# Performance work log

Hardware: AMD Instinct MI355X
Metric: run time of the kernel (lower is better)

Reference implementation:

```python
import jax, jax.numpy as jnp
import numpy as np

N = 50000      # nodes
E = 640000     # edges
F_IN = 128     # dataset.num_features
DIM = 128      # mParams['dim']
NC = 6         # dataset.num_classes
BN_EPS = 1e-5


def _bn_eval(z, g, b, rm, rv):
    return g * (z - rm) * jax.lax.rsqrt(rv + BN_EPS) + b


def _gin_layer(h, src, dst, W1, b1, g, be, rm, rv, W2, b2):
    # GINConv (eps=0): nn(x + sum_{j->i} x_j); messages from src aggregated at dst
    agg = jax.ops.segment_sum(h[src], dst, num_segments=N)
    z = (h + agg) @ W1 + b1
    z = jax.nn.relu(_bn_eval(z, g, be, rm, rv))
    z = jax.nn.relu(z @ W2 + b2)
    return z


def setup_inputs() -> dict:
    key = jax.random.key(0)
    ks = jax.random.split(key, 10)
    s = 1.0 / np.sqrt(DIM)
    inp = {
        'x': jax.random.normal(ks[0], (N, F_IN), jnp.float32),
        'edge_index': jax.random.randint(ks[1], (2, E), 0, N, dtype=jnp.int32),
        'batch': jnp.zeros((N,), jnp.int32),
        # conv1 MLP: Linear(F_IN,DIM) -> BN(DIM) -> ReLU -> Linear(DIM,DIM) -> ReLU
        'c1_W1': jax.random.normal(ks[2], (F_IN, DIM), jnp.float32) * s,
        'c1_b1': jnp.zeros((DIM,), jnp.float32),
        'c1_g': jnp.ones((DIM,), jnp.float32),
        'c1_beta': jnp.zeros((DIM,), jnp.float32),
        'c1_rm': jnp.zeros((DIM,), jnp.float32),
        'c1_rv': jnp.ones((DIM,), jnp.float32),
        'c1_W2': jax.random.normal(ks[3], (DIM, DIM), jnp.float32) * s,
        'c1_b2': jnp.zeros((DIM,), jnp.float32),
        # 2 extra GINConv layers (c_depth-1), stacked on leading axis
        'conv_W1': jax.random.normal(ks[4], (2, DIM, DIM), jnp.float32) * s,
        'conv_b1': jnp.zeros((2, DIM), jnp.float32),
        'conv_g': jnp.ones((2, DIM), jnp.float32),
        'conv_beta': jnp.zeros((2, DIM), jnp.float32),
        'conv_rm': jnp.zeros((2, DIM), jnp.float32),
        'conv_rv': jnp.ones((2, DIM), jnp.float32),
        'conv_W2': jax.random.normal(ks[5], (2, DIM, DIM), jnp.float32) * s,
        'conv_b2': jnp.zeros((2, DIM), jnp.float32),
        # 2 linear layers (l_depth)
        'lin_W': jax.random.normal(ks[6], (2, DIM, DIM), jnp.float32) * s,
        'lin_b': jnp.zeros((2, DIM), jnp.float32),
        # classifier Linear(2*DIM, NC)
        'cls_W': jax.random.normal(ks[7], (2 * DIM, NC), jnp.float32) * s,
        'cls_b': jnp.zeros((NC,), jnp.float32),
    }
    return inp


def reference(x, edge_index, batch,
              c1_W1, c1_b1, c1_g, c1_beta, c1_rm, c1_rv, c1_W2, c1_b2,
              conv_W1, conv_b1, conv_g, conv_beta, conv_rm, conv_rv, conv_W2, conv_b2,
              lin_W, lin_b, cls_W, cls_b):
    src, dst = edge_index[0], edge_index[1]
    h = _gin_layer(x, src, dst, c1_W1, c1_b1, c1_g, c1_beta, c1_rm, c1_rv, c1_W2, c1_b2)
    h = jax.nn.relu(h)  # extra .relu() after conv1 (idempotent)
    for i in range(conv_W1.shape[0]):
        h = _gin_layer(h, src, dst, conv_W1[i], conv_b1[i], conv_g[i], conv_beta[i],
                       conv_rm[i], conv_rv[i], conv_W2[i], conv_b2[i])
        h = jax.nn.relu(h)
    for i in range(lin_W.shape[0]):
        h = jax.nn.relu(h @ lin_W[i] + lin_b[i])
    # dropout: eval mode -> identity
    e = jnp.concatenate([h[src], h[dst]], axis=1)  # [E, 2*DIM]
    out = e @ cls_W + cls_b                         # [E, NC]
    return (out, e)
```

## Files before the change

kernel.cpp:

```cpp
#include <hip/hip_runtime.h>
#include <cstddef>
#include <cstdint>

#define NN 50000
#define EE 640000
#define FD 128


__global__ __launch_bounds__(256) void k_zero(int* __restrict__ p) {
  int i = blockIdx.x * 256 + threadIdx.x;
  if (i < NN) p[i] = 0;
}

__global__ __launch_bounds__(256) void k_hist(const int* __restrict__ dst,
                                              int* __restrict__ deg) {
  int e = blockIdx.x * 256 + threadIdx.x;
  atomicAdd(&deg[dst[e]], 1);
}

__global__ __launch_bounds__(1024) void k_scan(const int* __restrict__ deg,
                                               int* __restrict__ off,
                                               int* __restrict__ cur) {
  __shared__ int wsum[16], woff[16];
  __shared__ int carryS;
  const int t = threadIdx.x, lane = t & 63, w = t >> 6;
  if (t == 0) carryS = 0;
  __syncthreads();
  for (int base = 0; base < NN; base += 4096) {
    int i = base + (t << 2);
    int4 dv = make_int4(0, 0, 0, 0);
    if (i < NN) dv = *reinterpret_cast<const int4*>(deg + i);
    int tsum = dv.x + dv.y + dv.z + dv.w;
    int incl = tsum;
#pragma unroll
    for (int d = 1; d < 64; d <<= 1) {
      int u = __shfl_up(incl, d, 64);
      if (lane >= d) incl += u;
    }
    if (lane == 63) wsum[w] = incl;
    __syncthreads();
    if (t == 0) {
      int run = 0;
#pragma unroll
      for (int k = 0; k < 16; ++k) { woff[k] = run; run += wsum[k]; }
    }
    __syncthreads();
    int ebase = (incl - tsum) + woff[w] + carryS;
    if (i < NN) {
      int4 ov;
      ov.x = ebase;
      ov.y = ebase + dv.x;
      ov.z = ov.y + dv.y;
      ov.w = ov.z + dv.z;
      *reinterpret_cast<int4*>(off + i) = ov;
      *reinterpret_cast<int4*>(cur + i) = ov;
    }
    __syncthreads();
    if (t == 0) carryS += woff[15] + wsum[15];
    __syncthreads();
  }
}

__global__ __launch_bounds__(256) void k_fill(const int* __restrict__ src,
                                              const int* __restrict__ dst,
                                              int* __restrict__ cur,
                                              int* __restrict__ ssrc) {
  int e = blockIdx.x * 256 + threadIdx.x;
  int d = dst[e];
  int pos = atomicAdd(&cur[d], 1);
  ssrc[pos] = src[e];
}

__global__ __launch_bounds__(256) void k_agg(const float* __restrict__ h,
                                             const int* __restrict__ off,
                                             const int* __restrict__ deg,
                                             const int* __restrict__ ssrc,
                                             float* __restrict__ agg) {
  int node = blockIdx.x * 8 + (threadIdx.x >> 5);
  int lane = threadIdx.x & 31;
  int f = lane << 2;
  float4 acc = *reinterpret_cast<const float4*>(h + (size_t)node * FD + f);
  int n = deg[node];
  const int* sl = ssrc + off[node];
  int j = 0;
  for (; j + 4 <= n; j += 4) {
    int s0 = sl[j], s1 = sl[j + 1], s2 = sl[j + 2], s3 = sl[j + 3];
    float4 v0 = *reinterpret_cast<const float4*>(h + (size_t)s0 * FD + f);
    float4 v1 = *reinterpret_cast<const float4*>(h + (size_t)s1 * FD + f);
    float4 v2 = *reinterpret_cast<const float4*>(h + (size_t)s2 * FD + f);
    float4 v3 = *reinterpret_cast<const float4*>(h + (size_t)s3 * FD + f);
    acc.x += (v0.x + v1.x) + (v2.x + v3.x);
    acc.y += (v0.y + v1.y) + (v2.y + v3.y);
    acc.z += (v0.z + v1.z) + (v2.z + v3.z);
    acc.w += (v0.w + v1.w) + (v2.w + v3.w);
  }
  for (; j < n; ++j) {
    int s = sl[j];
    float4 v = *reinterpret_cast<const float4*>(h + (size_t)s * FD + f);
    acc.x += v.x; acc.y += v.y; acc.z += v.z; acc.w += v.w;
  }
  *reinterpret_cast<float4*>(agg + (size_t)node * FD + f) = acc;
}

__global__ __launch_bounds__(256) void k_gemm(const float* __restrict__ A,
                                              const float* __restrict__ W,
                                              const float* __restrict__ bias,
                                              const float* __restrict__ gg,
                                              const float* __restrict__ bb,
                                              const float* __restrict__ rm,
                                              const float* __restrict__ rv,
                                              int use_bn,
                                              float* __restrict__ O, int M) {
  __shared__ float At[64][68];
  __shared__ float Ws[64][132];
  const int t  = threadIdx.x;
  const int tx = t & 15;
  const int ty = t >> 4;
  const int rowBase = blockIdx.x * 64;

  float acc[4][8] = {};

  for (int kc = 0; kc < 2; ++kc) {
    const int k0 = kc * 64;
#pragma unroll
    for (int i = 0; i < 4; ++i) {
      int idx = t + i * 256;
      int row = idx >> 4;
      int kg  = (idx & 15) << 2;
      int r = rowBase + row;
      float4 v = make_float4(0.f, 0.f, 0.f, 0.f);
      if (r < M) v = *reinterpret_cast<const float4*>(A + (size_t)r * FD + k0 + kg);
      At[kg + 0][row] = v.x;
      At[kg + 1][row] = v.y;
      At[kg + 2][row] = v.z;
      At[kg + 3][row] = v.w;
    }
#pragma unroll
    for (int i = 0; i < 8; ++i) {
      int idx = t + i * 256;
      int wr = idx >> 5;
      int wc = (idx & 31) << 2;
      *reinterpret_cast<float4*>(&Ws[wr][wc]) =
          *reinterpret_cast<const float4*>(W + (size_t)(k0 + wr) * FD + wc);
    }
    __syncthreads();

#pragma unroll 8
    for (int k = 0; k < 64; ++k) {
      const float4 a  = *reinterpret_cast<const float4*>(&At[k][ty << 2]);
      const float4 w0 = *reinterpret_cast<const float4*>(&Ws[k][tx << 3]);
      const float4 w1 = *reinterpret_cast<const float4*>(&Ws[k][(tx << 3) + 4]);
      const float av[4] = {a.x, a.y, a.z, a.w};
      const float wv[8] = {w0.x, w0.y, w0.z, w0.w, w1.x, w1.y, w1.z, w1.w};
#pragma unroll
      for (int i = 0; i < 4; ++i)
#pragma unroll
        for (int j = 0; j < 8; ++j)
          acc[i][j] = fmaf(av[i], wv[j], acc[i][j]);
    }
    __syncthreads();
  }

  const int c0 = tx << 3;
  float sc[8], sh[8];
#pragma unroll
  for (int j = 0; j < 8; ++j) {
    int c = c0 + j;
    if (use_bn) {
      float s = gg[c] * rsqrtf(rv[c] + 1e-5f);
      sc[j] = s;
      sh[j] = (bias[c] - rm[c]) * s + bb[c];
    } else {
      sc[j] = 1.f;
      sh[j] = bias[c];
    }
  }
#pragma unroll
  for (int i = 0; i < 4; ++i) {
    int r = rowBase + (ty << 2) + i;
    if (r < M) {
      float o[8];
#pragma unroll
      for (int j = 0; j < 8; ++j) {
        float v = fmaf(acc[i][j], sc[j], sh[j]);
        o[j] = v > 0.f ? v : 0.f;
      }
      *reinterpret_cast<float4*>(O + (size_t)r * FD + c0) =
          make_float4(o[0], o[1], o[2], o[3]);
      *reinterpret_cast<float4*>(O + (size_t)r * FD + c0 + 4) =
          make_float4(o[4], o[5], o[6], o[7]);
    }
  }
}

__global__ __launch_bounds__(256) void k_uv(const float* __restrict__ h,
                                            const float* __restrict__ clsW,
                                            float* __restrict__ U,
                                            float* __restrict__ V) {
  int t = blockIdx.x * 256 + threadIdx.x;
  int r = t / 12;
  int c = t % 12;
  if (r >= NN) return;
  int cc = (c < 6) ? c : c - 6;
  int base = (c < 6) ? 0 : FD;
  const float* hr = h + (size_t)r * FD;
  float acc = 0.f;
#pragma unroll 8
  for (int k = 0; k < FD; ++k)
    acc = fmaf(hr[k], clsW[(size_t)(base + k) * 6 + cc], acc);
  if (c < 6) U[(size_t)r * 6 + cc] = acc;
  else       V[(size_t)r * 6 + cc] = acc;
}

__global__ __launch_bounds__(256) void k_edge(const float* __restrict__ h,
                                              const int* __restrict__ src,
                                              const int* __restrict__ dst,
                                              const float* __restrict__ U,
                                              const float* __restrict__ V,
                                              const float* __restrict__ clsB,
                                              float* __restrict__ outL,
                                              float* __restrict__ outE) {
  int eid  = blockIdx.x * 4 + (threadIdx.x >> 6);
  int lane = threadIdx.x & 63;
  int s = src[eid];
  int d = dst[eid];
  int node = (lane < 32) ? s : d;
  int f = (lane & 31) << 2;
  float4 v = *reinterpret_cast<const float4*>(h + (size_t)node * FD + f);
  *reinterpret_cast<float4*>(outE + (size_t)eid * 256 + (lane << 2)) = v;
  if (lane < 6)
    outL[(size_t)eid * 6 + lane] = U[(size_t)s * 6 + lane] + V[(size_t)d * 6 + lane] + clsB[lane];
}

extern "C" void kernel_launch(void* const* d_in, const int* in_sizes, int n_in,
                              void* d_out, int out_size, void* d_ws, size_t ws_size,
                              hipStream_t stream) {
  const float* x     = (const float*)d_in[0];
  const int*   ei    = (const int*)d_in[1];
  const int*   src   = ei;
  const int*   dst   = ei + EE;
  const float* c1_W1 = (const float*)d_in[3];
  const float* c1_b1 = (const float*)d_in[4];
  const float* c1_g  = (const float*)d_in[5];
  const float* c1_be = (const float*)d_in[6];
  const float* c1_rm = (const float*)d_in[7];
  const float* c1_rv = (const float*)d_in[8];
  const float* c1_W2 = (const float*)d_in[9];
  const float* c1_b2 = (const float*)d_in[10];
  const float* cv_W1 = (const float*)d_in[11];
  const float* cv_b1 = (const float*)d_in[12];
  const float* cv_g  = (const float*)d_in[13];
  const float* cv_be = (const float*)d_in[14];
  const float* cv_rm = (const float*)d_in[15];
  const float* cv_rv = (const float*)d_in[16];
  const float* cv_W2 = (const float*)d_in[17];
  const float* cv_b2 = (const float*)d_in[18];
  const float* ln_W  = (const float*)d_in[19];
  const float* ln_b  = (const float*)d_in[20];
  const float* clsW  = (const float*)d_in[21];
  const float* clsB  = (const float*)d_in[22];

  float* buf0 = (float*)d_ws;
  float* buf1 = buf0 + (size_t)NN * FD;
  float* Uu   = buf1 + (size_t)NN * FD;
  float* Vv   = Uu + (size_t)NN * 6;

  float* outL = (float*)d_out;
  float* outE = outL + (size_t)EE * 6;

  const size_t outFloats = (size_t)EE * 262;
  const size_t scrInts   = (size_t)NN * 3 + (size_t)EE;
  const size_t scrStart  = (outFloats - scrInts) & ~(size_t)3;
  int* deg  = (int*)d_out + scrStart;
  int* off  = deg + NN;
  int* curp = off + NN;
  int* ssrc = curp + NN;

  dim3 B(256);
  const int gZero = (NN + 255) / 256;
  const int gEdgeWk = EE / 256;
  const int gAgg  = NN / 8;
  const int gGemm = (NN + 63) / 64;
  const int gUV   = (NN * 12 + 255) / 256;
  const int gEdge = EE / 4;

  k_zero<<<gZero, B, 0, stream>>>(deg);
  k_hist<<<gEdgeWk, B, 0, stream>>>(dst, deg);
  k_scan<<<1, dim3(1024), 0, stream>>>(deg, off, curp);
  k_fill<<<gEdgeWk, B, 0, stream>>>(src, dst, curp, ssrc);

  float* bufs[2] = {buf0, buf1};

  k_agg<<<gAgg, B, 0, stream>>>(x, off, deg, ssrc, buf0);
  k_gemm<<<gGemm, B, 0, stream>>>(buf0, c1_W1, c1_b1, c1_g, c1_be, c1_rm, c1_rv, 1, buf1, NN);
  k_gemm<<<gGemm, B, 0, stream>>>(buf1, c1_W2, c1_b2, nullptr, nullptr, nullptr, nullptr, 0, buf0, NN);
  int pp = 0;

  for (int l = 0; l < 2; ++l) {
    float* hc = bufs[pp];
    float* ho = bufs[1 - pp];
    k_agg<<<gAgg, B, 0, stream>>>(hc, off, deg, ssrc, ho);
    k_gemm<<<gGemm, B, 0, stream>>>(ho, cv_W1 + (size_t)l * FD * FD, cv_b1 + l * FD,
                                    cv_g + l * FD, cv_be + l * FD, cv_rm + l * FD,
                                    cv_rv + l * FD, 1, hc, NN);
    k_gemm<<<gGemm, B, 0, stream>>>(hc, cv_W2 + (size_t)l * FD * FD, cv_b2 + l * FD,
                                    nullptr, nullptr, nullptr, nullptr, 0, ho, NN);
    pp = 1 - pp;
  }

  for (int l = 0; l < 2; ++l) {
    k_gemm<<<gGemm, B, 0, stream>>>(bufs[pp], ln_W + (size_t)l * FD * FD, ln_b + l * FD,
                                    nullptr, nullptr, nullptr, nullptr, 0, bufs[1 - pp], NN);
    pp = 1 - pp;
  }

  k_uv<<<gUV, B, 0, stream>>>(bufs[pp], clsW, Uu, Vv);
  k_edge<<<gEdge, B, 0, stream>>>(bufs[pp], src, dst, Uu, Vv, clsB, outL, outE);
}
```

Measured before the change: 1.428 ms.

## Retile GEMM to 128-row blocks, warp-reduce classifier, unroll aggregation, nontemporal edge stores

The GEMM block tile grows from 64 to 128 rows with 8x8 register tiles per thread and 32-wide k chunks, which raises arithmetic intensity per shared-memory load. The U/V classifier projection now uses 32 lanes per node with coalesced float4 row reads and a shuffle reduction, replacing one thread per output that read the whole row serially. The aggregation loop gains an 8-way unrolled gather to put more loads in flight, and the large edge-feature output is written with nontemporal stores to reduce cache pollution. The larger register tile may lower occupancy, and the gather-heavy kernels remain limited by memory bandwidth.

```diff
diff --git a/kernel.cpp b/kernel.cpp
--- a/kernel.cpp
+++ b/kernel.cpp
@@ -5,6 +5,8 @@
 #define NN 50000
 #define EE 640000
 #define FD 128
+
+typedef float fvec4 __attribute__((ext_vector_type(4)));
 
 
 __global__ __launch_bounds__(256) void k_zero(int* __restrict__ p) {
@@ -83,6 +85,27 @@
   int n = deg[node];
   const int* sl = ssrc + off[node];
   int j = 0;
+  for (; j + 8 <= n; j += 8) {
+    int s0 = sl[j], s1 = sl[j + 1], s2 = sl[j + 2], s3 = sl[j + 3];
+    int s4 = sl[j + 4], s5 = sl[j + 5], s6 = sl[j + 6], s7 = sl[j + 7];
+    float4 v0 = *reinterpret_cast<const float4*>(h + (size_t)s0 * FD + f);
+    float4 v1 = *reinterpret_cast<const float4*>(h + (size_t)s1 * FD + f);
+    float4 v2 = *reinterpret_cast<const float4*>(h + (size_t)s2 * FD + f);
+    float4 v3 = *reinterpret_cast<const float4*>(h + (size_t)s3 * FD + f);
+    float4 v4 = *reinterpret_cast<const float4*>(h + (size_t)s4 * FD + f);
+    float4 v5 = *reinterpret_cast<const float4*>(h + (size_t)s5 * FD + f);
+    float4 v6 = *reinterpret_cast<const float4*>(h + (size_t)s6 * FD + f);
+    float4 v7 = *reinterpret_cast<const float4*>(h + (size_t)s7 * FD + f);
+    float tx0 = (v0.x + v1.x) + (v2.x + v3.x);
+    float ty0 = (v0.y + v1.y) + (v2.y + v3.y);
+    float tz0 = (v0.z + v1.z) + (v2.z + v3.z);
+    float tw0 = (v0.w + v1.w) + (v2.w + v3.w);
+    float tx1 = (v4.x + v5.x) + (v6.x + v7.x);
+    float ty1 = (v4.y + v5.y) + (v6.y + v7.y);
+    float tz1 = (v4.z + v5.z) + (v6.z + v7.z);
+    float tw1 = (v4.w + v5.w) + (v6.w + v7.w);
+    acc.x += tx0 + tx1; acc.y += ty0 + ty1; acc.z += tz0 + tz1; acc.w += tw0 + tw1;
+  }
   for (; j + 4 <= n; j += 4) {
     int s0 = sl[j], s1 = sl[j + 1], s2 = sl[j + 2], s3 = sl[j + 3];
     float4 v0 = *reinterpret_cast<const float4*>(h + (size_t)s0 * FD + f);
@@ -111,22 +134,22 @@
                                               const float* __restrict__ rv,
                                               int use_bn,
                                               float* __restrict__ O, int M) {
-  __shared__ float At[64][68];
-  __shared__ float Ws[64][132];
+  __shared__ float At[32][132];
+  __shared__ float Ws[32][132];
   const int t  = threadIdx.x;
   const int tx = t & 15;
   const int ty = t >> 4;
-  const int rowBase = blockIdx.x * 64;
-
-  float acc[4][8] = {};
-
-  for (int kc = 0; kc < 2; ++kc) {
-    const int k0 = kc * 64;
+  const int rowBase = blockIdx.x * 128;
+
+  float acc[8][8] = {};
+
+  for (int kc = 0; kc < 4; ++kc) {
+    const int k0 = kc << 5;
 #pragma unroll
     for (int i = 0; i < 4; ++i) {
-      int idx = t + i * 256;
-      int row = idx >> 4;
-      int kg  = (idx & 15) << 2;
+      int fl = t + (i << 8);
+      int row = fl & 127;
+      int kg  = (fl >> 7) << 2;
       int r = rowBase + row;
       float4 v = make_float4(0.f, 0.f, 0.f, 0.f);
       if (r < M) v = *reinterpret_cast<const float4*>(A + (size_t)r * FD + k0 + kg);
@@ -136,36 +159,36 @@
       At[kg + 3][row] = v.w;
     }
 #pragma unroll
-    for (int i = 0; i < 8; ++i) {
-      int idx = t + i * 256;
-      int wr = idx >> 5;
-      int wc = (idx & 31) << 2;
+    for (int i = 0; i < 4; ++i) {
+      int fl = t + (i << 8);
+      int wr = fl >> 5;
+      int wc = (fl & 31) << 2;
       *reinterpret_cast<float4*>(&Ws[wr][wc]) =
           *reinterpret_cast<const float4*>(W + (size_t)(k0 + wr) * FD + wc);
     }
     __syncthreads();
 
 #pragma unroll 8
-    for (int k = 0; k < 64; ++k) {
-      const float4 a  = *reinterpret_cast<const float4*>(&At[k][ty << 2]);
-      const float4 w0 = *reinterpret_cast<const float4*>(&Ws[k][tx << 3]);
-      const float4 w1 = *reinterpret_cast<const float4*>(&Ws[k][(tx << 3) + 4]);
-      const float av[4] = {a.x, a.y, a.z, a.w};
+    for (int k = 0; k < 32; ++k) {
+      const float4 a0 = *reinterpret_cast<const float4*>(&At[k][ty << 3]);
+      const float4 a1 = *reinterpret_cast<const float4*>(&At[k][(ty << 3) + 4]);
+      const float4 w0 = *reinterpret_cast<const float4*>(&Ws[k][tx << 2]);
+      const float4 w1 = *reinterpret_cast<const float4*>(&Ws[k][64 + (tx << 2)]);
+      const float av[8] = {a0.x, a0.y, a0.z, a0.w, a1.x, a1.y, a1.z, a1.w};
       const float wv[8] = {w0.x, w0.y, w0.z, w0.w, w1.x, w1.y, w1.z, w1.w};
 #pragma unroll
-      for (int i = 0; i < 4; ++i)
+      for (int i2 = 0; i2 < 8; ++i2)
 #pragma unroll
         for (int j = 0; j < 8; ++j)
-          acc[i][j] = fmaf(av[i], wv[j], acc[i][j]);
-    }
-    __syncthreads();
-  }
-
-  const int c0 = tx << 3;
+          acc[i2][j] = fmaf(av[i2], wv[j], acc[i2][j]);
+    }
+    __syncthreads();
+  }
+
   float sc[8], sh[8];
 #pragma unroll
   for (int j = 0; j < 8; ++j) {
-    int c = c0 + j;
+    int c = (j < 4) ? ((tx << 2) + j) : (64 + (tx << 2) + (j - 4));
     if (use_bn) {
       float s = gg[c] * rsqrtf(rv[c] + 1e-5f);
       sc[j] = s;
@@ -176,8 +199,8 @@
     }
   }
 #pragma unroll
-  for (int i = 0; i < 4; ++i) {
-    int r = rowBase + (ty << 2) + i;
+  for (int i = 0; i < 8; ++i) {
+    int r = rowBase + (ty << 3) + i;
     if (r < M) {
       float o[8];
 #pragma unroll
@@ -185,9 +208,9 @@
         float v = fmaf(acc[i][j], sc[j], sh[j]);
         o[j] = v > 0.f ? v : 0.f;
       }
-      *reinterpret_cast<float4*>(O + (size_t)r * FD + c0) =
+      *reinterpret_cast<float4*>(O + (size_t)r * FD + (tx << 2)) =
           make_float4(o[0], o[1], o[2], o[3]);
-      *reinterpret_cast<float4*>(O + (size_t)r * FD + c0 + 4) =
+      *reinterpret_cast<float4*>(O + (size_t)r * FD + 64 + (tx << 2)) =
           make_float4(o[4], o[5], o[6], o[7]);
     }
   }
@@ -197,19 +220,32 @@
                                             const float* __restrict__ clsW,
                                             float* __restrict__ U,
                                             float* __restrict__ V) {
-  int t = blockIdx.x * 256 + threadIdx.x;
-  int r = t / 12;
-  int c = t % 12;
-  if (r >= NN) return;
-  int cc = (c < 6) ? c : c - 6;
-  int base = (c < 6) ? 0 : FD;
-  const float* hr = h + (size_t)r * FD;
-  float acc = 0.f;
-#pragma unroll 8
-  for (int k = 0; k < FD; ++k)
-    acc = fmaf(hr[k], clsW[(size_t)(base + k) * 6 + cc], acc);
-  if (c < 6) U[(size_t)r * 6 + cc] = acc;
-  else       V[(size_t)r * 6 + cc] = acc;
+  int node = blockIdx.x * 8 + (threadIdx.x >> 5);
+  int lane = threadIdx.x & 31;
+  int f = lane << 2;
+  float4 v = *reinterpret_cast<const float4*>(h + (size_t)node * FD + f);
+  float p[12];
+#pragma unroll
+  for (int c = 0; c < 6; ++c) {
+    p[c] = fmaf(v.x, clsW[(size_t)(f + 0) * 6 + c],
+           fmaf(v.y, clsW[(size_t)(f + 1) * 6 + c],
+           fmaf(v.z, clsW[(size_t)(f + 2) * 6 + c],
+                v.w * clsW[(size_t)(f + 3) * 6 + c])));
+    p[6 + c] = fmaf(v.x, clsW[(size_t)(FD + f + 0) * 6 + c],
+               fmaf(v.y, clsW[(size_t)(FD + f + 1) * 6 + c],
+               fmaf(v.z, clsW[(size_t)(FD + f + 2) * 6 + c],
+                    v.w * clsW[(size_t)(FD + f + 3) * 6 + c])));
+  }
+#pragma unroll
+  for (int m = 16; m >= 1; m >>= 1) {
+#pragma unroll
+    for (int c = 0; c < 12; ++c) p[c] += __shfl_xor(p[c], m, 64);
+  }
+  float outv = 0.f;
+#pragma unroll
+  for (int c = 0; c < 12; ++c) outv = (lane == c) ? p[c] : outv;
+  if (lane < 6)       U[(size_t)node * 6 + lane] = outv;
+  else if (lane < 12) V[(size_t)node * 6 + (lane - 6)] = outv;
 }
 
 __global__ __launch_bounds__(256) void k_edge(const float* __restrict__ h,
@@ -226,10 +262,12 @@
   int d = dst[eid];
   int node = (lane < 32) ? s : d;
   int f = (lane & 31) << 2;
-  float4 v = *reinterpret_cast<const float4*>(h + (size_t)node * FD + f);
-  *reinterpret_cast<float4*>(outE + (size_t)eid * 256 + (lane << 2)) = v;
-  if (lane < 6)
-    outL[(size_t)eid * 6 + lane] = U[(size_t)s * 6 + lane] + V[(size_t)d * 6 + lane] + clsB[lane];
+  fvec4 v = *reinterpret_cast<const fvec4*>(h + (size_t)node * FD + f);
+  __builtin_nontemporal_store(v, reinterpret_cast<fvec4*>(outE + (size_t)eid * 256 + (lane << 2)));
+  if (lane < 6) {
+    float lv = U[(size_t)s * 6 + lane] + V[(size_t)d * 6 + lane] + clsB[lane];
+    __builtin_nontemporal_store(lv, outL + (size_t)eid * 6 + lane);
+  }
 }
 
 extern "C" void kernel_launch(void* const* d_in, const int* in_sizes, int n_in,
@@ -277,12 +315,12 @@
   int* ssrc = curp + NN;
 
   dim3 B(256);
-  const int gZero = (NN + 255) / 256;
+  const int gZero   = (NN + 255) / 256;
   const int gEdgeWk = EE / 256;
-  const int gAgg  = NN / 8;
-  const int gGemm = (NN + 63) / 64;
-  const int gUV   = (NN * 12 + 255) / 256;
-  const int gEdge = EE / 4;
+  const int gAgg    = NN / 8;
+  const int gGemm   = (NN + 127) / 128;
+  const int gUV     = NN / 8;
+  const int gEdge   = EE / 4;
 
   k_zero<<<gZero, B, 0, stream>>>(deg);
   k_hist<<<gEdgeWk, B, 0, stream>>>(dst, deg);
```

New measurement: 1.284 ms. 10.1% less time.
